# Performance work log

Hardware: AMD Instinct MI355X
Metric: run time of the kernel (lower is better)

## Reference

```python
import jax, jax.numpy as jnp
import numpy as np

D_MODEL = 1024
HEADS = 16
D_HEAD = D_MODEL // HEADS


def setup_inputs() -> dict:
    key = jax.random.key(0)
    ks = jax.random.split(key, 12)
    B, L = 2, 2048
    s = 1.0 / np.sqrt(D_MODEL)
    inp = {
        "q": jax.random.normal(ks[0], (B, L, D_MODEL), jnp.float32),
        "k": jax.random.normal(ks[1], (B, L, D_MODEL), jnp.float32),
        "v": jax.random.normal(ks[2], (B, L, D_MODEL), jnp.float32),
        # torch nn.Linear params: weight [out, in], bias [out]
        "w_q": jax.random.normal(ks[3], (D_MODEL, D_MODEL), jnp.float32) * s,
        "b_q": jax.random.normal(ks[4], (D_MODEL,), jnp.float32) * s,
        "w_k": jax.random.normal(ks[5], (D_MODEL, D_MODEL), jnp.float32) * s,
        "b_k": jax.random.normal(ks[6], (D_MODEL,), jnp.float32) * s,
        "w_v": jax.random.normal(ks[7], (D_MODEL, D_MODEL), jnp.float32) * s,
        "b_v": jax.random.normal(ks[8], (D_MODEL,), jnp.float32) * s,
        "w_o": jax.random.normal(ks[9], (D_MODEL, D_MODEL), jnp.float32) * s,
        "b_o": jax.random.normal(ks[10], (D_MODEL,), jnp.float32) * s,
    }
    return inp


def reference(q, k, v, w_q, b_q, w_k, b_k, w_v, b_v, w_o, b_o):
    B, L, _ = q.shape
    # QKV projections (torch Linear: x @ W^T + b)
    qh = (q @ w_q.T + b_q).reshape(B, L, HEADS, D_HEAD)
    kh = (k @ w_k.T + b_k).reshape(B, L, HEADS, D_HEAD)
    vh = (v @ w_v.T + b_v).reshape(B, L, HEADS, D_HEAD)
    # scaled dot-product attention per head
    scale = 1.0 / jnp.sqrt(jnp.asarray(D_HEAD, qh.dtype))
    scores = jnp.einsum("bqhd,bkhd->bhqk", qh, kh) * scale  # [B,H,Lq,Lk]
    attn = jax.nn.softmax(scores, axis=-1)
    out = jnp.einsum("bhqk,bkhd->bqhd", attn, vh)  # [B,Lq,H,Dh]
    out = out.reshape(B, L, HEADS * D_HEAD)
    return out @ w_o.T + b_o
```

## Files before the change

kernel.cpp:

```cpp
#include <hip/hip_runtime.h>
#include <hip/hip_bf16.h>

typedef __attribute__((ext_vector_type(8))) short bf16x8;
typedef __attribute__((ext_vector_type(2))) float f32x2;
typedef __attribute__((ext_vector_type(4))) float f32x4;
typedef __attribute__((ext_vector_type(16))) float f32x16;
typedef __attribute__((ext_vector_type(2))) unsigned u32x2;
typedef __attribute__((ext_vector_type(4))) unsigned u32x4;
typedef __attribute__((ext_vector_type(4))) float float4a;

#define DEV static __device__ __forceinline__

constexpr int DM = 1024;
constexpr int NH = 16;
constexpr int DH = 64;
constexpr int BATCH = 2;
constexpr int SEQ = 2048;
constexpr int NROWS = BATCH * NH * SEQ;
constexpr float CS = 0.18033688011112042f;

DEV unsigned short f2bf(float x) {
  unsigned u = __float_as_uint(x);
  u += 0x7fff + ((u >> 16) & 1);
  return (unsigned short)(u >> 16);
}
DEV float bf2f(short h) {
  unsigned u = ((unsigned)(unsigned short)h) << 16;
  return __uint_as_float(u);
}
DEV unsigned pk2(float a, float b) {
  return (unsigned)f2bf(a) | ((unsigned)f2bf(b) << 16);
}
DEV unsigned pkrn(float a, float b) {
  union { __hip_bfloat162 h; unsigned u; } cv;
  cv.h = __float22bfloat162_rn(make_float2(a, b));
  return cv.u;
}

DEV void gload16(const void* g, void* l) {
  __builtin_amdgcn_global_load_lds(
      (const __attribute__((address_space(1))) unsigned*)g,
      (__attribute__((address_space(3))) unsigned*)l, 16, 0, 0);
}

DEV u32x2 plswap(unsigned a, unsigned b) {
  auto r = __builtin_amdgcn_permlane32_swap(a, b, false, false);
  return (u32x2){(unsigned)r[0], (unsigned)r[1]};
}
DEV float xsum32(float x) {
  u32x2 r = plswap(__float_as_uint(x), __float_as_uint(x));
  return __uint_as_float(r[0]) + __uint_as_float(r[1]);
}

DEV float tree16(const f32x16& v) {
  f32x2 a0 = {v[0], v[1]},  a1 = {v[2], v[3]},  a2 = {v[4], v[5]},  a3 = {v[6], v[7]};
  f32x2 a4 = {v[8], v[9]},  a5 = {v[10], v[11]}, a6 = {v[12], v[13]}, a7 = {v[14], v[15]};
  f32x2 b0 = a0 + a1, b1 = a2 + a3, b2 = a4 + a5, b3 = a6 + a7;
  f32x2 c0 = b0 + b1, c1 = b2 + b3;
  f32x2 d = c0 + c1;
  return d[0] + d[1];
}

__global__ void cvt7_kernel(const float* s0, const float* s1, const float* s2,
                            const float* s3, const float* s4, const float* s5, const float* s6,
                            short* d0, short* d1, short* d2, short* d3,
                            short* d4, short* d5, short* d6) {
  const float* s; short* d; int n8;
  switch (blockIdx.z) {
    case 0: s = s0; d = d0; n8 = 524288; break;
    case 1: s = s1; d = d1; n8 = 524288; break;
    case 2: s = s2; d = d2; n8 = 524288; break;
    case 3: s = s3; d = d3; n8 = 131072; break;
    case 4: s = s4; d = d4; n8 = 131072; break;
    case 5: s = s5; d = d5; n8 = 131072; break;
    default: s = s6; d = d6; n8 = 131072; break;
  }
  int i = blockIdx.x * blockDim.x + threadIdx.x;
  if (i >= n8) return;
  const float4a* sp = (const float4a*)s;
  float4a a = sp[2 * i], b = sp[2 * i + 1];
  bf16x8 o;
  o[0] = (short)f2bf(a[0]); o[1] = (short)f2bf(a[1]);
  o[2] = (short)f2bf(a[2]); o[3] = (short)f2bf(a[3]);
  o[4] = (short)f2bf(b[0]); o[5] = (short)f2bf(b[1]);
  o[6] = (short)f2bf(b[2]); o[7] = (short)f2bf(b[3]);
  ((bf16x8*)d)[i] = o;
}

template<int OUTF32>
__global__ __launch_bounds__(256, 2)
void gemm_bias(const short* __restrict__ A0, const short* __restrict__ A1, const short* __restrict__ A2,
               const short* __restrict__ W0, const short* __restrict__ W1, const short* __restrict__ W2,
               const float* __restrict__ bi0, const float* __restrict__ bi1, const float* __restrict__ bi2,
               void* C0, void* C1, void* C2,
               int M, int N, int K) {
  const short* A = A0; const short* W = W0; const float* bias = bi0; void* C = C0;
  if (blockIdx.z == 1) { A = A1; W = W1; bias = bi1; C = C1; }
  if (blockIdx.z == 2) { A = A2; W = W2; bias = bi2; C = C2; }

  __shared__ short sA[128 * 64];
  __shared__ short sB[128 * 64];

  const int t = threadIdx.x;
  const int lane = t & 63;
  const int w = t >> 6;
  const int wm = w >> 1, wn = w & 1;
  const int m0 = blockIdx.y * 128;
  const int n0 = blockIdx.x * 128;

  f32x4 acc[4][4] = {};

  const int srow = t >> 3;
  const int schk = t & 7;

  for (int k0 = 0; k0 < K; k0 += 64) {
    __syncthreads();
#pragma unroll
    for (int r = 0; r < 4; ++r) {
      int row = r * 32 + srow;
      int cl = schk ^ (row & 7);
      gload16(A + (size_t)(m0 + row) * K + k0 + cl * 8,
              (char*)sA + r * 4096 + w * 1024);
      gload16(W + (size_t)(n0 + row) * K + k0 + cl * 8,
              (char*)sB + r * 4096 + w * 1024);
    }
    __syncthreads();
#pragma unroll
    for (int ks = 0; ks < 2; ++ks) {
      bf16x8 af[4], bfr[4];
#pragma unroll
      for (int f = 0; f < 4; ++f) {
        int ra = wm * 64 + f * 16 + (lane & 15);
        int ca = (ks * 4 + (lane >> 4)) ^ (ra & 7);
        af[f] = *(const bf16x8*)((const char*)sA + ra * 128 + ca * 16);
        int rb = wn * 64 + f * 16 + (lane & 15);
        int cb2 = (ks * 4 + (lane >> 4)) ^ (rb & 7);
        bfr[f] = *(const bf16x8*)((const char*)sB + rb * 128 + cb2 * 16);
      }
#pragma unroll
      for (int mf = 0; mf < 4; ++mf)
#pragma unroll
        for (int nf = 0; nf < 4; ++nf)
          acc[mf][nf] = __builtin_amdgcn_mfma_f32_16x16x32_bf16(af[mf], bfr[nf], acc[mf][nf], 0, 0, 0);
    }
  }

  const int cb = n0 + wn * 64 + (lane & 15);
  const int rb = m0 + wm * 64 + ((lane >> 4) << 2);
  const float sc = (OUTF32 == 0 && blockIdx.z == 0) ? CS : 1.0f;
  if (OUTF32 == 0 && blockIdx.z == 2) {
#pragma unroll
    for (int nf = 0; nf < 4; ++nf) {
      float bv = bias[cb + nf * 16];
#pragma unroll
      for (int mf = 0; mf < 4; ++mf) {
        u32x2 pr;
        pr[0] = pk2(acc[mf][nf][0] + bv, acc[mf][nf][1] + bv);
        pr[1] = pk2(acc[mf][nf][2] + bv, acc[mf][nf][3] + bv);
        *(u32x2*)((short*)C + (size_t)(cb + nf * 16) * M + rb + mf * 16) = pr;
      }
    }
  } else {
#pragma unroll
    for (int nf = 0; nf < 4; ++nf) {
      float bv = bias[cb + nf * 16];
#pragma unroll
      for (int mf = 0; mf < 4; ++mf) {
#pragma unroll
        for (int j = 0; j < 4; ++j) {
          float vv = (acc[mf][nf][j] + bv) * sc;
          size_t idx = (size_t)(rb + mf * 16 + j) * N + cb + nf * 16;
          if (OUTF32) ((float*)C)[idx] = vv;
          else        ((short*)C)[idx] = (short)f2bf(vv);
        }
      }
    }
  }
}

__global__ __launch_bounds__(256, 4)
void attn_kernel(const short* __restrict__ qh, const short* __restrict__ kh,
                 const short* __restrict__ vt,
                 short* __restrict__ po0, short* __restrict__ po1,
                 float* __restrict__ pl) {
  const int bh = blockIdx.y;
  const int b = bh >> 4, h = bh & 15;
  const int q0 = blockIdx.x * 128;
  const int sp = blockIdx.z;
  const int kvbase = sp * (SEQ / 2);
  const int t = threadIdx.x;
  const int lane = t & 63;
  const int w = t >> 6;
  const int hi = lane >> 5, l31 = lane & 31;

  __shared__ short sK[2][4096];
  __shared__ short sVt[2][4096];

  bf16x8 qf[4];
  {
    const short* qp = qh + ((size_t)b * SEQ + q0 + w * 32 + l31) * DM + h * DH + hi * 8;
#pragma unroll
    for (int ks = 0; ks < 4; ++ks) qf[ks] = *(const bf16x8*)(qp + ks * 16);
  }

  f32x16 o0 = {}, o1 = {};
  float l = 0.f;

  const short* kB = kh + ((size_t)b * SEQ) * DM + h * DH;
  const short* vtB = vt + (size_t)(h * DH) * (BATCH * SEQ) + b * SEQ;

  int c_row[2], c_off[2];
#pragma unroll
  for (int half = 0; half < 2; ++half) {
    int c = half * 256 + t;
    c_row[half] = c >> 3;
    c_off[half] = ((c & 7) ^ ((c >> 3) & 7)) * 8;
  }

  auto stage = [&](int buf, int kv0) {
#pragma unroll
    for (int half = 0; half < 2; ++half) {
      gload16(kB + (size_t)(kv0 + c_row[half]) * DM + c_off[half],
              (char*)&sK[buf][0] + half * 4096 + w * 1024);
      gload16(vtB + (size_t)c_row[half] * (BATCH * SEQ) + kv0 + c_off[half],
              (char*)&sVt[buf][0] + half * 4096 + w * 1024);
    }
  };

  stage(0, kvbase);
  __syncthreads();

  constexpr int NT = (SEQ / 2) / 64;
  for (int tt = 0; tt < NT; ++tt) {
    const int cur = tt & 1;
    if (tt + 1 < NT) stage(cur ^ 1, kvbase + (tt + 1) * 64);

    f32x16 s0 = {}, s1 = {};
    {
      const char* kbase = (const char*)&sK[cur][0];
      __builtin_amdgcn_s_setprio(1);
#pragma unroll
      for (int ks = 0; ks < 4; ++ks) {
        int ch = ((ks * 2 + hi) ^ (l31 & 7)) * 16;
        bf16x8 a0 = *(const bf16x8*)(kbase + l31 * 128 + ch);
        bf16x8 a1 = *(const bf16x8*)(kbase + (32 + l31) * 128 + ch);
        s0 = __builtin_amdgcn_mfma_f32_32x32x16_bf16(a0, qf[ks], s0, 0, 0, 0);
        s1 = __builtin_amdgcn_mfma_f32_32x32x16_bf16(a1, qf[ks], s1, 0, 0, 0);
      }
      __builtin_amdgcn_s_setprio(0);
    }

#pragma unroll
    for (int r = 0; r < 16; ++r) s0[r] = exp2f(s0[r]);
#pragma unroll
    for (int r = 0; r < 16; ++r) s1[r] = exp2f(s1[r]);
    l += tree16(s0) + tree16(s1);

    union U { u32x4 u; bf16x8 h; };
    bf16x8 pa[4];
#pragma unroll
    for (int ks = 0; ks < 4; ++ks) {
      const f32x16 sv = (ks < 2) ? s0 : s1;
      const int ro = (ks & 1) * 8;
      unsigned u0 = pkrn(sv[ro + 0], sv[ro + 1]);
      unsigned u1 = pkrn(sv[ro + 2], sv[ro + 3]);
      unsigned u2 = pkrn(sv[ro + 4], sv[ro + 5]);
      unsigned u3 = pkrn(sv[ro + 6], sv[ro + 7]);
      u32x2 r02 = plswap(u0, u2);
      u32x2 r13 = plswap(u1, u3);
      U pu;
      pu.u = (u32x4){r02[0], r13[0], r02[1], r13[1]};
      pa[ks] = pu.h;
    }

    {
      const char* vbase = (const char*)&sVt[cur][0];
      __builtin_amdgcn_s_setprio(1);
#pragma unroll
      for (int ks = 0; ks < 4; ++ks) {
        int ch = ((ks * 2 + hi) ^ (l31 & 7)) * 16;
        bf16x8 vb0 = *(const bf16x8*)(vbase + l31 * 128 + ch);
        bf16x8 vb1 = *(const bf16x8*)(vbase + (32 + l31) * 128 + ch);
        o0 = __builtin_amdgcn_mfma_f32_32x32x16_bf16(pa[ks], vb0, o0, 0, 0, 0);
        o1 = __builtin_amdgcn_mfma_f32_32x32x16_bf16(pa[ks], vb1, o1, 0, 0, 0);
      }
      __builtin_amdgcn_s_setprio(0);
    }

    __syncthreads();
  }

  const int rowbase = bh * SEQ + q0 + w * 32;
  float lt = xsum32(l);
  if (lane < 32) pl[sp * NROWS + rowbase + lane] = lt;
  short* pb = sp ? po1 : po0;
#pragma unroll
  for (int r = 0; r < 16; ++r) {
    int qr = (r & 3) + 8 * (r >> 2) + 4 * hi;
    size_t base = (size_t)(rowbase + qr) * 64 + l31;
    pb[base]      = (short)f2bf(o0[r]);
    pb[base + 32] = (short)f2bf(o1[r]);
  }
}

__global__ void combine_kernel(const short* __restrict__ po0, const short* __restrict__ po1,
                               const float* __restrict__ pl,
                               short* __restrict__ ao) {
  int idx = blockIdx.x * 256 + threadIdx.x;
  int row = idx >> 3, d8 = (idx & 7) * 8;
  float inv = 1.0f / (pl[row] + pl[NROWS + row]);
  bf16x8 a = *(const bf16x8*)(po0 + (size_t)row * 64 + d8);
  bf16x8 b = *(const bf16x8*)(po1 + (size_t)row * 64 + d8);
  int bh = row >> 11, q = row & 2047;
  int bb = bh >> 4, hh = bh & 15;
  short* dst = ao + ((size_t)bb * SEQ + q) * DM + hh * DH + d8;
  bf16x8 o;
#pragma unroll
  for (int e = 0; e < 8; ++e)
    o[e] = (short)f2bf((bf2f(a[e]) + bf2f(b[e])) * inv);
  *(bf16x8*)dst = o;
}

extern "C" void kernel_launch(void* const* d_in, const int* in_sizes, int n_in,
                              void* d_out, int out_size, void* d_ws, size_t ws_size,
                              hipStream_t stream) {
  (void)in_sizes; (void)n_in; (void)out_size; (void)ws_size;
  const float* q   = (const float*)d_in[0];
  const float* k   = (const float*)d_in[1];
  const float* v   = (const float*)d_in[2];
  const float* w_q = (const float*)d_in[3];
  const float* b_q = (const float*)d_in[4];
  const float* w_k = (const float*)d_in[5];
  const float* b_k = (const float*)d_in[6];
  const float* w_v = (const float*)d_in[7];
  const float* b_v = (const float*)d_in[8];
  const float* w_o = (const float*)d_in[9];
  const float* b_o = (const float*)d_in[10];

  char* ws = (char*)d_ws;
  const size_t MB = 1u << 20;
  short* qb  = (short*)(ws + 0 * MB);
  short* kb  = (short*)(ws + 8 * MB);
  short* vb  = (short*)(ws + 16 * MB);
  short* wqb = (short*)(ws + 24 * MB);
  short* wkb = (short*)(ws + 26 * MB);
  short* wvb = (short*)(ws + 28 * MB);
  short* wob = (short*)(ws + 30 * MB);
  short* qhb = (short*)(ws + 32 * MB);
  short* khb = (short*)(ws + 40 * MB);
  short* vtb = (short*)(ws + 48 * MB);
  short* aob = (short*)(ws + 56 * MB);
  short* po0 = (short*)(ws + 0 * MB);
  short* po1 = (short*)(ws + 8 * MB);
  float* pl  = (float*)(ws + 16 * MB);

  dim3 gc(2048, 1, 7);
  cvt7_kernel<<<gc, 256, 0, stream>>>(q, k, v, w_q, w_k, w_v, w_o,
                                      qb, kb, vb, wqb, wkb, wvb, wob);

  dim3 gq(1024 / 128, 4096 / 128, 3);
  gemm_bias<0><<<gq, 256, 0, stream>>>(qb, kb, vb, wqb, wkb, wvb,
                                       b_q, b_k, b_v, qhb, khb, vtb,
                                       4096, 1024, 1024);

  dim3 ga(SEQ / 128, BATCH * NH, 2);
  attn_kernel<<<ga, 256, 0, stream>>>(qhb, khb, vtb, po0, po1, pl);

  combine_kernel<<<(NROWS * 8) / 256, 256, 0, stream>>>(po0, po1, pl, aob);

  dim3 go(1024 / 128, 4096 / 128, 1);
  gemm_bias<1><<<go, 256, 0, stream>>>(aob, aob, aob, wob, wob, wob,
                                       b_o, b_o, b_o, d_out, d_out, d_out,
                                       4096, 1024, 1024);
}
```

Baseline: 141.7 us.

## Use 512-thread attention blocks over 256 query rows with a 4-way KV split

The attention kernel now runs 8 waves per block covering 256 query rows, so each staged K/V tile is shared by twice as many waves and each thread issues one async load per tile instead of two. The KV sequence is split four ways instead of two, which keeps the total grid size unchanged and shortens each block's loop. The combine kernel now sums four bf16 partial outputs and four row-sum partials, adding read traffic. Workspace buffers are remapped onto regions that are no longer live at that point.

```diff
diff --git a/kernel.cpp b/kernel.cpp
--- a/kernel.cpp
+++ b/kernel.cpp
@@ -178,16 +178,17 @@
   }
 }
 
-__global__ __launch_bounds__(256, 4)
+__global__ __launch_bounds__(512, 8)
 void attn_kernel(const short* __restrict__ qh, const short* __restrict__ kh,
                  const short* __restrict__ vt,
                  short* __restrict__ po0, short* __restrict__ po1,
+                 short* __restrict__ po2, short* __restrict__ po3,
                  float* __restrict__ pl) {
   const int bh = blockIdx.y;
   const int b = bh >> 4, h = bh & 15;
-  const int q0 = blockIdx.x * 128;
+  const int q0 = blockIdx.x * 256;
   const int sp = blockIdx.z;
-  const int kvbase = sp * (SEQ / 2);
+  const int kvbase = sp * (SEQ / 4);
   const int t = threadIdx.x;
   const int lane = t & 63;
   const int w = t >> 6;
@@ -209,28 +210,20 @@
   const short* kB = kh + ((size_t)b * SEQ) * DM + h * DH;
   const short* vtB = vt + (size_t)(h * DH) * (BATCH * SEQ) + b * SEQ;
 
-  int c_row[2], c_off[2];
-#pragma unroll
-  for (int half = 0; half < 2; ++half) {
-    int c = half * 256 + t;
-    c_row[half] = c >> 3;
-    c_off[half] = ((c & 7) ^ ((c >> 3) & 7)) * 8;
-  }
+  const int c_row = t >> 3;
+  const int c_off = ((t & 7) ^ ((t >> 3) & 7)) * 8;
 
   auto stage = [&](int buf, int kv0) {
-#pragma unroll
-    for (int half = 0; half < 2; ++half) {
-      gload16(kB + (size_t)(kv0 + c_row[half]) * DM + c_off[half],
-              (char*)&sK[buf][0] + half * 4096 + w * 1024);
-      gload16(vtB + (size_t)c_row[half] * (BATCH * SEQ) + kv0 + c_off[half],
-              (char*)&sVt[buf][0] + half * 4096 + w * 1024);
-    }
+    gload16(kB + (size_t)(kv0 + c_row) * DM + c_off,
+            (char*)&sK[buf][0] + w * 1024);
+    gload16(vtB + (size_t)c_row * (BATCH * SEQ) + kv0 + c_off,
+            (char*)&sVt[buf][0] + w * 1024);
   };
 
   stage(0, kvbase);
   __syncthreads();
 
-  constexpr int NT = (SEQ / 2) / 64;
+  constexpr int NT = (SEQ / 4) / 64;
   for (int tt = 0; tt < NT; ++tt) {
     const int cur = tt & 1;
     if (tt + 1 < NT) stage(cur ^ 1, kvbase + (tt + 1) * 64);
@@ -293,7 +286,7 @@
   const int rowbase = bh * SEQ + q0 + w * 32;
   float lt = xsum32(l);
   if (lane < 32) pl[sp * NROWS + rowbase + lane] = lt;
-  short* pb = sp ? po1 : po0;
+  short* pb = (sp & 2) ? ((sp & 1) ? po3 : po2) : ((sp & 1) ? po1 : po0);
 #pragma unroll
   for (int r = 0; r < 16; ++r) {
     int qr = (r & 3) + 8 * (r >> 2) + 4 * hi;
@@ -304,20 +297,23 @@
 }
 
 __global__ void combine_kernel(const short* __restrict__ po0, const short* __restrict__ po1,
+                               const short* __restrict__ po2, const short* __restrict__ po3,
                                const float* __restrict__ pl,
                                short* __restrict__ ao) {
   int idx = blockIdx.x * 256 + threadIdx.x;
   int row = idx >> 3, d8 = (idx & 7) * 8;
-  float inv = 1.0f / (pl[row] + pl[NROWS + row]);
+  float inv = 1.0f / (pl[row] + pl[NROWS + row] + pl[2 * NROWS + row] + pl[3 * NROWS + row]);
   bf16x8 a = *(const bf16x8*)(po0 + (size_t)row * 64 + d8);
   bf16x8 b = *(const bf16x8*)(po1 + (size_t)row * 64 + d8);
+  bf16x8 c = *(const bf16x8*)(po2 + (size_t)row * 64 + d8);
+  bf16x8 d = *(const bf16x8*)(po3 + (size_t)row * 64 + d8);
   int bh = row >> 11, q = row & 2047;
   int bb = bh >> 4, hh = bh & 15;
   short* dst = ao + ((size_t)bb * SEQ + q) * DM + hh * DH + d8;
   bf16x8 o;
 #pragma unroll
   for (int e = 0; e < 8; ++e)
-    o[e] = (short)f2bf((bf2f(a[e]) + bf2f(b[e])) * inv);
+    o[e] = (short)f2bf(((bf2f(a[e]) + bf2f(b[e])) + (bf2f(c[e]) + bf2f(d[e]))) * inv);
   *(bf16x8*)dst = o;
 }
 
@@ -349,10 +345,12 @@
   short* qhb = (short*)(ws + 32 * MB);
   short* khb = (short*)(ws + 40 * MB);
   short* vtb = (short*)(ws + 48 * MB);
-  short* aob = (short*)(ws + 56 * MB);
   short* po0 = (short*)(ws + 0 * MB);
   short* po1 = (short*)(ws + 8 * MB);
-  float* pl  = (float*)(ws + 16 * MB);
+  short* po2 = (short*)(ws + 16 * MB);
+  short* po3 = (short*)(ws + 56 * MB);
+  float* pl  = (float*)(ws + 24 * MB);
+  short* aob = (short*)(ws + 32 * MB);
 
   dim3 gc(2048, 1, 7);
   cvt7_kernel<<<gc, 256, 0, stream>>>(q, k, v, w_q, w_k, w_v, w_o,
@@ -363,10 +361,10 @@
                                        b_q, b_k, b_v, qhb, khb, vtb,
                                        4096, 1024, 1024);
 
-  dim3 ga(SEQ / 128, BATCH * NH, 2);
-  attn_kernel<<<ga, 256, 0, stream>>>(qhb, khb, vtb, po0, po1, pl);
-
-  combine_kernel<<<(NROWS * 8) / 256, 256, 0, stream>>>(po0, po1, pl, aob);
+  dim3 ga(SEQ / 256, BATCH * NH, 4);
+  attn_kernel<<<ga, 512, 0, stream>>>(qhb, khb, vtb, po0, po1, po2, po3, pl);
+
+  combine_kernel<<<(NROWS * 8) / 256, 256, 0, stream>>>(po0, po1, po2, po3, pl, aob);
 
   dim3 go(1024 / 128, 4096 / 128, 1);
   gemm_bias<1><<<go, 256, 0, stream>>>(aob, aob, aob, wob, wob, wob,
```

New measurement: 404.0 us. +185.2%, slower.
